# Optimization experiments

Measured on AMD Instinct MI355X. Metric: run time of the kernel, lower is better.

## Reference

```python
import jax, jax.numpy as jnp
import numpy as np

EMBED_DIM = 1024
NUM_HEADS = 16
HEAD_DIM = EMBED_DIM // NUM_HEADS
MAX_LEN = 1000  # default in RelativePositionalEncoding
B, T = 4, 1024


def setup_inputs() -> dict:
    key = jax.random.key(0)
    ks = jax.random.split(key, 12)
    s = 0.02
    d = EMBED_DIM
    return {
        "query": jax.random.normal(ks[0], (B, T, d), jnp.float32),
        "key": jax.random.normal(ks[1], (B, T, d), jnp.float32),
        "value": jax.random.normal(ks[2], (B, T, d), jnp.float32),
        "Wq": jax.random.normal(ks[3], (d, d), jnp.float32) * s,
        "bq": jnp.zeros((d,), jnp.float32),
        "Wk": jax.random.normal(ks[4], (d, d), jnp.float32) * s,
        "bk": jnp.zeros((d,), jnp.float32),
        "Wv": jax.random.normal(ks[5], (d, d), jnp.float32) * s,
        "bv": jnp.zeros((d,), jnp.float32),
        "Wo": jax.random.normal(ks[6], (d, d), jnp.float32) * s,
        "bo": jnp.zeros((d,), jnp.float32),
        "rel_emb": jax.random.normal(ks[7], (2 * MAX_LEN - 1, HEAD_DIM), jnp.float32) * s,
    }


def reference(query, key, value, Wq, bq, Wk, bk, Wv, bv, Wo, bo, rel_emb):
    Bq, Tq, C = query.shape
    H, hd = NUM_HEADS, HEAD_DIM
    # projections -> [B, H, T, hd]
    q = (query @ Wq.T + bq).reshape(Bq, Tq, H, hd).transpose(0, 2, 1, 3)
    k = (key @ Wk.T + bk).reshape(Bq, Tq, H, hd).transpose(0, 2, 1, 3)
    v = (value @ Wv.T + bv).reshape(Bq, Tq, H, hd).transpose(0, 2, 1, 3)
    # content scores [B, H, T, T]
    attn_scores = jnp.einsum('bhtd,bhsd->bhts', q, k)
    # relative positional embedding gather: E[t, s] = rel_emb[clamp(s - t + max_len - 1)]
    pos = jnp.arange(Tq)
    idx = jnp.clip(pos[None, :] - pos[:, None] + MAX_LEN - 1, 0, 2 * MAX_LEN - 2)
    E = rel_emb[idx]  # [T, T, hd]
    # NOTE: original uses raw (unprojected) query reshaped into heads for rel-pos scores
    rpe_q = query.transpose(1, 0, 2).reshape(Tq, Bq * H, hd)  # [T, B*H, hd]
    rpe = jnp.einsum('tnd,tsd->nts', rpe_q, E).reshape(Bq, H, Tq, Tq)
    # faithful to original: divide by scale = hd**-0.5 (i.e. multiply by sqrt(hd))
    scale = hd ** (-0.5)
    attn = (attn_scores + rpe) / scale
    attn_weights = jax.nn.softmax(attn, axis=-1)
    out = jnp.einsum('bhts,bhsd->bhtd', attn_weights, v)
    out = out.transpose(0, 2, 1, 3).reshape(Bq, Tq, C)
    return out @ Wo.T + bo
```

## Files before the change

kernel.cpp:

```cpp
#include <hip/hip_runtime.h>
#include <math.h>

typedef _Float16 h16;
typedef __attribute__((ext_vector_type(4))) _Float16 half4;
typedef __attribute__((ext_vector_type(8))) _Float16 half8;
typedef __attribute__((ext_vector_type(4))) float f32x4;

#define AS1 __attribute__((address_space(1)))
#define AS3 __attribute__((address_space(3)))
#define MFMA16(a, b, c) __builtin_amdgcn_mfma_f32_16x16x32_f16((a), (b), (c), 0, 0, 0)

__device__ __forceinline__ float ex2(float x) {
  return __builtin_amdgcn_exp2f(x);
}

template <int CTRL>
__device__ __forceinline__ float dppf(float x) {
  return __int_as_float(__builtin_amdgcn_update_dpp(
      0, __float_as_int(x), CTRL, 0xF, 0xF, true));
}
__device__ __forceinline__ float rmax16(float x) {
  x = fmaxf(x, dppf<0xB1>(x));
  x = fmaxf(x, dppf<0x4E>(x));
  x = fmaxf(x, dppf<0x124>(x));
  x = fmaxf(x, dppf<0x128>(x));
  return x;
}
__device__ __forceinline__ float rsum16(float x) {
  x += dppf<0xB1>(x);
  x += dppf<0x4E>(x);
  x += dppf<0x124>(x);
  x += dppf<0x128>(x);
  return x;
}

__global__ __launch_bounds__(256) void convert(
    const float* __restrict__ q, const float* __restrict__ k,
    const float* __restrict__ v, const float* __restrict__ Wq,
    const float* __restrict__ Wk, const float* __restrict__ Wv,
    const float* __restrict__ Wo, const float* __restrict__ rel, h16* q16c,
    h16* k16c, h16* v16c, h16* Wq16, h16* Wk16, h16* Wv16, h16* Wo16,
    h16* relb) {
  const int i = blockIdx.x * 256 + threadIdx.x;
  if (i >= 4226304) return;
  const float* src;
  h16* dst;
  int off;
  if (i < 1048576) {
    src = q; dst = q16c; off = i;
  } else if (i < 2097152) {
    src = k; dst = k16c; off = i - 1048576;
  } else if (i < 3145728) {
    src = v; dst = v16c; off = i - 2097152;
  } else if (i < 3407872) {
    src = Wq; dst = Wq16; off = i - 3145728;
  } else if (i < 3670016) {
    src = Wk; dst = Wk16; off = i - 3407872;
  } else if (i < 3932160) {
    src = Wv; dst = Wv16; off = i - 3670016;
  } else if (i < 4194304) {
    src = Wo; dst = Wo16; off = i - 3932160;
  } else {
    off = i - 4194304;
    half4 hv = (half4){(h16)0.f, (h16)0.f, (h16)0.f, (h16)0.f};
    if (off < 31984) {
      float4 f = *(const float4*)(rel + (size_t)off * 4);
      hv = (half4){(h16)f.x, (h16)f.y, (h16)f.z, (h16)f.w};
    }
    *(half4*)(relb + (size_t)off * 4) = hv;
    return;
  }
  float4 f = *(const float4*)(src + (size_t)off * 4);
  *(half4*)(dst + (size_t)off * 4) =
      (half4){(h16)f.x, (h16)f.y, (h16)f.z, (h16)f.w};
}

template <int MODE>
__device__ __forceinline__ void gemm128_body(const h16* __restrict__ A,
                                             const h16* __restrict__ Bt,
                                             const float* __restrict__ bias,
                                             h16* __restrict__ outp) {
  __shared__ alignas(16) h16 As[128 * 64];
  __shared__ alignas(16) h16 Bs[128 * 64];
  const int tid = threadIdx.x;
  const int wave = tid >> 6;
  const int lane = tid & 63;
  const int wm = wave >> 1, wn = wave & 1;
  const int tm0 = blockIdx.x * 128, tn0 = blockIdx.y * 128;
  const int lrow = lane & 15;
  const int kq = lane >> 4;

  f32x4 acc[4][4];
#pragma unroll
  for (int i = 0; i < 4; ++i)
#pragma unroll
    for (int j = 0; j < 4; ++j) acc[i][j] = (f32x4){0.f, 0.f, 0.f, 0.f};

  for (int k0 = 0; k0 < 1024; k0 += 64) {
    __syncthreads();
#pragma unroll
    for (int p = 0; p < 4; ++p) {
      const int a = (wave * 4 + p) * 64 + lane;
      const int row = a >> 3;
      const int c = (a & 7) ^ (row & 7);
      __builtin_amdgcn_global_load_lds(
          (const AS1 void*)(A + (size_t)(tm0 + row) * 1024 + k0 + c * 8),
          (AS3 void*)(As + (wave * 4 + p) * 512), 16, 0, 0);
      __builtin_amdgcn_global_load_lds(
          (const AS1 void*)(Bt + (size_t)(tn0 + row) * 1024 + k0 + c * 8),
          (AS3 void*)(Bs + (wave * 4 + p) * 512), 16, 0, 0);
    }
    __syncthreads();
#pragma unroll
    for (int ks2 = 0; ks2 < 2; ++ks2) {
      const int cu = ((ks2 * 4 + kq) ^ (lrow & 7)) << 3;
      half8 af[4], bf[4];
#pragma unroll
      for (int i = 0; i < 4; ++i)
        af[i] = *(const half8*)(As + (wm * 64 + i * 16 + lrow) * 64 + cu);
#pragma unroll
      for (int j = 0; j < 4; ++j)
        bf[j] = *(const half8*)(Bs + (wn * 64 + j * 16 + lrow) * 64 + cu);
#pragma unroll
      for (int i = 0; i < 4; ++i)
#pragma unroll
        for (int j = 0; j < 4; ++j)
          acc[i][j] = MFMA16(af[i], bf[j], acc[i][j]);
    }
  }

#pragma unroll
  for (int j = 0; j < 4; ++j) {
    const int n = tn0 + wn * 64 + j * 16 + lrow;
    const float bval = bias[n];
#pragma unroll
    for (int i = 0; i < 4; ++i) {
      const int rowb = wm * 64 + i * 16 + (lane >> 4) * 4;
#pragma unroll
      for (int r = 0; r < 4; ++r) {
        const int m = tm0 + rowb + r;
        const float val = acc[i][j][r] + bval;
        const int b = m >> 10, t = m & 1023, hh = n >> 6, d = n & 63;
        if (MODE == 0) {
          outp[((size_t)((b << 4) + hh) << 16) + (t << 6) + d] = (h16)val;
        } else {
          outp[(((size_t)((b << 4) + hh) * 64 + d) << 10) + t] = (h16)val;
        }
      }
    }
  }
}

__global__ __launch_bounds__(256) void qkv_gemm(
    const h16* q16c, const h16* k16c, const h16* v16c, const h16* Wq16,
    const h16* Wk16, const h16* Wv16, const float* bq, const float* bk,
    const float* bv, h16* q16, h16* k16, h16* vt16) {
  const int z = blockIdx.z;
  const h16* A = (z == 0) ? q16c : (z == 1) ? k16c : v16c;
  const h16* Bt = (z == 0) ? Wq16 : (z == 1) ? Wk16 : Wv16;
  const float* bias = (z == 0) ? bq : (z == 1) ? bk : bv;
  if (z == 2)
    gemm128_body<1>(A, Bt, bias, vt16);
  else
    gemm128_body<0>(A, Bt, bias, (z == 0) ? q16 : k16);
}

__global__ __launch_bounds__(256) void out_gemm(const h16* __restrict__ A,
                                                const h16* __restrict__ Bt,
                                                const float* __restrict__ bo,
                                                float* __restrict__ out) {
  __shared__ alignas(16) h16 As[64 * 64];
  __shared__ alignas(16) h16 Bs[128 * 64];
  const int tid = threadIdx.x;
  const int wave = tid >> 6;
  const int lane = tid & 63;
  const int wm = wave >> 1, wn = wave & 1;
  const int tm0 = blockIdx.x * 64, tn0 = blockIdx.y * 128;
  const int lrow = lane & 15;
  const int kq = lane >> 4;

  f32x4 acc[2][4];
#pragma unroll
  for (int i = 0; i < 2; ++i)
#pragma unroll
    for (int j = 0; j < 4; ++j) acc[i][j] = (f32x4){0.f, 0.f, 0.f, 0.f};

  for (int k0 = 0; k0 < 1024; k0 += 64) {
    __syncthreads();
#pragma unroll
    for (int p = 0; p < 2; ++p) {
      const int a = (wave * 2 + p) * 64 + lane;
      const int row = a >> 3;
      const int c = (a & 7) ^ (row & 7);
      __builtin_amdgcn_global_load_lds(
          (const AS1 void*)(A + (size_t)(tm0 + row) * 1024 + k0 + c * 8),
          (AS3 void*)(As + (wave * 2 + p) * 512), 16, 0, 0);
    }
#pragma unroll
    for (int p = 0; p < 4; ++p) {
      const int a = (wave * 4 + p) * 64 + lane;
      const int row = a >> 3;
      const int c = (a & 7) ^ (row & 7);
      __builtin_amdgcn_global_load_lds(
          (const AS1 void*)(Bt + (size_t)(tn0 + row) * 1024 + k0 + c * 8),
          (AS3 void*)(Bs + (wave * 4 + p) * 512), 16, 0, 0);
    }
    __syncthreads();
#pragma unroll
    for (int ks2 = 0; ks2 < 2; ++ks2) {
      const int cu = ((ks2 * 4 + kq) ^ (lrow & 7)) << 3;
      half8 af[2], bf[4];
#pragma unroll
      for (int i = 0; i < 2; ++i)
        af[i] = *(const half8*)(As + (wm * 32 + i * 16 + lrow) * 64 + cu);
#pragma unroll
      for (int j = 0; j < 4; ++j)
        bf[j] = *(const half8*)(Bs + (wn * 64 + j * 16 + lrow) * 64 + cu);
#pragma unroll
      for (int i = 0; i < 2; ++i)
#pragma unroll
        for (int j = 0; j < 4; ++j)
          acc[i][j] = MFMA16(af[i], bf[j], acc[i][j]);
    }
  }

#pragma unroll
  for (int j = 0; j < 4; ++j) {
    const int n = tn0 + wn * 64 + j * 16 + lrow;
    const float bval = bo[n];
#pragma unroll
    for (int i = 0; i < 2; ++i) {
      const int rowb = wm * 32 + i * 16 + kq * 4;
#pragma unroll
      for (int r = 0; r < 4; ++r) {
        const int m = tm0 + rowb + r;
        out[(size_t)m * 1024 + n] = acc[i][j][r] + bval;
      }
    }
  }
}

__global__ __launch_bounds__(256, 4) void attn_mfma(
    const h16* __restrict__ q16, const h16* __restrict__ k16,
    const h16* __restrict__ vt16, const h16* __restrict__ q16c,
    const h16* __restrict__ relb, h16* __restrict__ ao) {
  __shared__ alignas(16) h16 Kh[4096];
  __shared__ alignas(16) h16 Rl[8192];
  __shared__ alignas(16) h16 VtS[4096];
  __shared__ alignas(16) h16 Ps[4096];

  const int bid = blockIdx.x;
  const int ttile = bid & 15;
  const int bh = bid >> 4;
  const int b = bh >> 4, h = bh & 15;
  const int t0 = ttile << 6;
  const int tid = threadIdx.x;
  const int w = tid >> 6;
  const int lane = tid & 63;
  const int l15 = lane & 15;
  const int kq = lane >> 4;

  const int tq = t0 + w * 16 + l15;
  half8 aq[2], arq[2];
#pragma unroll
  for (int ks = 0; ks < 2; ++ks) {
    aq[ks] =
        *(const half8*)(q16 + ((size_t)bh * 1024 + tq) * 64 + kq * 8 + ks * 32);
    arq[ks] = *(const half8*)(q16c + ((size_t)(b * 1024 + tq)) * 1024 + h * 64 +
                              kq * 8 + ks * 32);
  }

  float m2[4], ls[4];
  f32x4 O[4];
#pragma unroll
  for (int r = 0; r < 4; ++r) {
    m2[r] = -1e30f;
    ls[r] = 0.f;
  }
#pragma unroll
  for (int db = 0; db < 4; ++db) O[db] = (f32x4){0.f, 0.f, 0.f, 0.f};

  const int trow = w * 16 + kq * 4;

  for (int s0 = 0; s0 < 1024; s0 += 64) {
    __syncthreads();

#pragma unroll
    for (int p = 0; p < 2; ++p) {
      const int a = (w * 2 + p) * 64 + lane;
      const int row = a >> 3;
      const int c = (a & 7) ^ (row & 7);
      __builtin_amdgcn_global_load_lds(
          (const AS1 void*)(k16 + ((size_t)(bh * 1024 + s0 + row)) * 64 +
                            c * 8),
          (AS3 void*)(Kh + (w * 2 + p) * 512), 16, 0, 0);
    }
#pragma unroll
    for (int p = 0; p < 2; ++p) {
      const int a = (w * 2 + p) * 64 + lane;
      const int row = a >> 3;
      const int c = (a & 7) ^ (row & 7);
      __builtin_amdgcn_global_load_lds(
          (const AS1 void*)(vt16 + ((size_t)(bh * 64 + row)) * 1024 + s0 +
                            c * 8),
          (AS3 void*)(VtS + (w * 2 + p) * 512), 16, 0, 0);
    }
    const int base = s0 - t0 + 999 - 63;
#pragma unroll
    for (int p = 0; p < 4; ++p) {
      const int a = (w * 4 + p) * 64 + lane;
      const int row = a >> 3;
      const int c = (a & 7) ^ (row & 7);
      int ridx = base + row;
      ridx = ridx < 0 ? 0 : (ridx > 1998 ? 1998 : ridx);
      __builtin_amdgcn_global_load_lds(
          (const AS1 void*)(relb + (size_t)ridx * 64 + c * 8),
          (AS3 void*)(Rl + (w * 4 + p) * 512), 16, 0, 0);
    }
    __syncthreads();

    __builtin_amdgcn_s_setprio(1);
    f32x4 S[4];
#pragma unroll
    for (int ns = 0; ns < 4; ++ns) {
      f32x4 s = (f32x4){0.f, 0.f, 0.f, 0.f};
      const int kr = ns * 16 + l15;
#pragma unroll
      for (int ks = 0; ks < 2; ++ks) {
        const int c = ((ks * 4 + kq) ^ (kr & 7)) << 3;
        s = MFMA16(aq[ks], *(const half8*)(Kh + kr * 64 + c), s);
      }
      S[ns] = s;
    }

    f32x4 G[5];
#pragma unroll
    for (int gi = 0; gi < 5; ++gi) {
      f32x4 g = (f32x4){0.f, 0.f, 0.f, 0.f};
      const int ur = (3 - w + gi) * 16 + l15;
#pragma unroll
      for (int ks = 0; ks < 2; ++ks) {
        const int c = ((ks * 4 + kq) ^ (ur & 7)) << 3;
        g = MFMA16(arq[ks], *(const half8*)(Rl + ur * 64 + c), g);
      }
      G[gi] = g;
    }
    __builtin_amdgcn_s_setprio(0);

    const float SC = 11.54156032711170727f;
#pragma unroll
    for (int r = 0; r < 4; ++r) {
      const int Cm = 15 - kq * 4 - r;
      const int sladdr = ((kq << 4) | ((l15 + Cm) & 15)) << 2;
      const bool nolap = (l15 >= Cm);
#pragma unroll
      for (int ns = 0; ns < 4; ++ns) {
        const float mv = nolap ? G[ns][r] : G[ns + 1][r];
        const float g = __int_as_float(
            __builtin_amdgcn_ds_bpermute(sladdr, __float_as_int(mv)));
        S[ns][r] = (S[ns][r] + g) * SC;
      }
    }

#pragma unroll
    for (int r = 0; r < 4; ++r) {
      float mx = fmaxf(fmaxf(S[0][r], S[1][r]), fmaxf(S[2][r], S[3][r]));
      mx = rmax16(mx);
      const float nm = fmaxf(m2[r], mx);
      const float al = ex2(m2[r] - nm);
      m2[r] = nm;
      const int t = trow + r;
      float rs = 0.f;
#pragma unroll
      for (int ns = 0; ns < 4; ++ns) {
        const float p = ex2(S[ns][r] - nm);
        rs += p;
        const int sl = ns * 16 + l15;
        Ps[t * 64 + (((sl >> 3) ^ (t & 7)) << 3) + (sl & 7)] = (h16)p;
      }
      rs = rsum16(rs);
      ls[r] = ls[r] * al + rs;
      O[0][r] *= al;
      O[1][r] *= al;
      O[2][r] *= al;
      O[3][r] *= al;
    }

    const int tp = w * 16 + l15;
    __builtin_amdgcn_s_setprio(1);
#pragma unroll
    for (int ks = 0; ks < 2; ++ks) {
      const int ca = ((ks * 4 + kq) ^ (tp & 7)) << 3;
      half8 pa = *(const half8*)(Ps + tp * 64 + ca);
#pragma unroll
      for (int db = 0; db < 4; ++db) {
        const int vr = db * 16 + l15;
        const int cb = ((ks * 4 + kq) ^ (vr & 7)) << 3;
        O[db] = MFMA16(pa, *(const half8*)(VtS + vr * 64 + cb), O[db]);
      }
    }
    __builtin_amdgcn_s_setprio(0);
  }

#pragma unroll
  for (int r = 0; r < 4; ++r) {
    const float inv = 1.f / ls[r];
    const int t = t0 + trow + r;
    h16* op = ao + ((size_t)(b * 1024 + t)) * 1024 + h * 64;
#pragma unroll
    for (int db = 0; db < 4; ++db) op[db * 16 + l15] = (h16)(O[db][r] * inv);
  }
}

extern "C" void kernel_launch(void* const* d_in, const int* in_sizes, int n_in,
                              void* d_out, int out_size, void* d_ws,
                              size_t ws_size, hipStream_t stream) {
  const float* query = (const float*)d_in[0];
  const float* key = (const float*)d_in[1];
  const float* value = (const float*)d_in[2];
  const float* Wq = (const float*)d_in[3];
  const float* bq = (const float*)d_in[4];
  const float* Wk = (const float*)d_in[5];
  const float* bk = (const float*)d_in[6];
  const float* Wv = (const float*)d_in[7];
  const float* bv = (const float*)d_in[8];
  const float* Wo = (const float*)d_in[9];
  const float* bo = (const float*)d_in[10];
  const float* rel = (const float*)d_in[11];

  char* ws = (char*)d_ws;
  h16* q16c = (h16*)ws;
  h16* k16c = (h16*)(ws + ((size_t)8 << 20));
  h16* v16c = (h16*)(ws + ((size_t)16 << 20));
  h16* Wq16 = (h16*)(ws + ((size_t)24 << 20));
  h16* Wk16 = (h16*)(ws + ((size_t)26 << 20));
  h16* Wv16 = (h16*)(ws + ((size_t)28 << 20));
  h16* Wo16 = (h16*)(ws + ((size_t)30 << 20));
  h16* q16 = (h16*)(ws + ((size_t)32 << 20));
  h16* k16 = (h16*)(ws + ((size_t)40 << 20));
  h16* vt16 = (h16*)(ws + ((size_t)48 << 20));
  h16* relb = (h16*)(ws + ((size_t)56 << 20));
  h16* ao = k16c;
  float* out = (float*)d_out;

  convert<<<16509, 256, 0, stream>>>(query, key, value, Wq, Wk, Wv, Wo, rel,
                                     q16c, k16c, v16c, Wq16, Wk16, Wv16, Wo16,
                                     relb);
  qkv_gemm<<<dim3(32, 8, 3), 256, 0, stream>>>(q16c, k16c, v16c, Wq16, Wk16,
                                               Wv16, bq, bk, bv, q16, k16,
                                               vt16);
  attn_mfma<<<1024, 256, 0, stream>>>(q16, k16, vt16, q16c, relb, ao);
  out_gemm<<<dim3(64, 8), 256, 0, stream>>>(ao, Wo16, bo, out);
}
```

Before: 252.7 us.

## Rewrite QKV GEMM as 256x256 double-buffered tile with interleaved prefetch

```diff
diff --git a/kernel.cpp b/kernel.cpp
--- a/kernel.cpp
+++ b/kernel.cpp
@@ -75,73 +75,109 @@
       (half4){(h16)f.x, (h16)f.y, (h16)f.z, (h16)f.w};
 }
 
-template <int MODE>
-__device__ __forceinline__ void gemm128_body(const h16* __restrict__ A,
-                                             const h16* __restrict__ Bt,
-                                             const float* __restrict__ bias,
-                                             h16* __restrict__ outp) {
-  __shared__ alignas(16) h16 As[128 * 64];
-  __shared__ alignas(16) h16 Bs[128 * 64];
+__global__ __launch_bounds__(512) void qkv_gemm(
+    const h16* q16c, const h16* k16c, const h16* v16c, const h16* Wq16,
+    const h16* Wk16, const h16* Wv16, const float* bq, const float* bk,
+    const float* bv, h16* q16, h16* k16, h16* vt16) {
+  __shared__ alignas(16) h16 AsB[2][16384];
+  __shared__ alignas(16) h16 BsB[2][16384];
+
+  const int z = blockIdx.z;
+  const h16* __restrict__ A = (z == 0) ? q16c : (z == 1) ? k16c : v16c;
+  const h16* __restrict__ Bt = (z == 0) ? Wq16 : (z == 1) ? Wk16 : Wv16;
+  const float* __restrict__ bias = (z == 0) ? bq : (z == 1) ? bk : bv;
+  h16* __restrict__ outp = (z == 0) ? q16 : (z == 1) ? k16 : vt16;
+  const int mode = (z == 2) ? 1 : 0;
+
   const int tid = threadIdx.x;
-  const int wave = tid >> 6;
+  const int w = tid >> 6;
   const int lane = tid & 63;
-  const int wm = wave >> 1, wn = wave & 1;
-  const int tm0 = blockIdx.x * 128, tn0 = blockIdx.y * 128;
-  const int lrow = lane & 15;
+  const int wm = w >> 2, wn = w & 3;
+  const int tm0 = blockIdx.x * 256, tn0 = blockIdx.y * 256;
+  const int l15 = lane & 15;
   const int kq = lane >> 4;
 
-  f32x4 acc[4][4];
-#pragma unroll
-  for (int i = 0; i < 4; ++i)
+  f32x4 acc[8][4];
+#pragma unroll
+  for (int i = 0; i < 8; ++i)
 #pragma unroll
     for (int j = 0; j < 4; ++j) acc[i][j] = (f32x4){0.f, 0.f, 0.f, 0.f};
 
-  for (int k0 = 0; k0 < 1024; k0 += 64) {
-    __syncthreads();
-#pragma unroll
-    for (int p = 0; p < 4; ++p) {
-      const int a = (wave * 4 + p) * 64 + lane;
-      const int row = a >> 3;
-      const int c = (a & 7) ^ (row & 7);
-      __builtin_amdgcn_global_load_lds(
-          (const AS1 void*)(A + (size_t)(tm0 + row) * 1024 + k0 + c * 8),
-          (AS3 void*)(As + (wave * 4 + p) * 512), 16, 0, 0);
-      __builtin_amdgcn_global_load_lds(
-          (const AS1 void*)(Bt + (size_t)(tn0 + row) * 1024 + k0 + c * 8),
-          (AS3 void*)(Bs + (wave * 4 + p) * 512), 16, 0, 0);
-    }
-    __syncthreads();
-#pragma unroll
-    for (int ks2 = 0; ks2 < 2; ++ks2) {
-      const int cu = ((ks2 * 4 + kq) ^ (lrow & 7)) << 3;
-      half8 af[4], bf[4];
-#pragma unroll
-      for (int i = 0; i < 4; ++i)
-        af[i] = *(const half8*)(As + (wm * 64 + i * 16 + lrow) * 64 + cu);
-#pragma unroll
-      for (int j = 0; j < 4; ++j)
-        bf[j] = *(const half8*)(Bs + (wn * 64 + j * 16 + lrow) * 64 + cu);
-#pragma unroll
-      for (int i = 0; i < 4; ++i)
-#pragma unroll
-        for (int j = 0; j < 4; ++j)
-          acc[i][j] = MFMA16(af[i], bf[j], acc[i][j]);
+  const auto stage_ht = [&](int b, int hq, int kt) {
+    const int k0 = kt * 64;
+    const h16* src = (hq < 2) ? A : Bt;
+    const int br = (hq < 2) ? tm0 : tn0;
+    h16* dst = ((hq < 2) ? AsB[b] : BsB[b]) + (hq & 1) * 8192;
+#pragma unroll
+    for (int p = 0; p < 2; ++p) {
+      const int u = (w * 2 + p) * 64 + lane;
+      const int row = (hq & 1) * 128 + (u >> 3);
+      const int c = (u & 7) ^ (row & 7);
+      __builtin_amdgcn_global_load_lds(
+          (const AS1 void*)(src + (size_t)(br + row) * 1024 + k0 + c * 8),
+          (AS3 void*)(dst + (w * 2 + p) * 512), 16, 0, 0);
+    }
+  };
+
+#pragma unroll
+  for (int hq = 0; hq < 4; ++hq) stage_ht(0, hq, 0);
+
+  for (int kt = 0; kt < 16; ++kt) {
+    asm volatile("s_waitcnt vmcnt(0)" ::: "memory");
+    __builtin_amdgcn_s_barrier();
+    const h16* As_ = AsB[kt & 1];
+    const h16* Bs_ = BsB[kt & 1];
+
+    half8 bf[4][2];
+#pragma unroll
+    for (int n = 0; n < 4; ++n)
+#pragma unroll
+      for (int kh = 0; kh < 2; ++kh) {
+        const int row = wn * 64 + n * 16 + l15;
+        const int cu = ((kh * 4 + kq) ^ (row & 7)) << 3;
+        bf[n][kh] = *(const half8*)(Bs_ + row * 64 + cu);
+      }
+
+#pragma unroll
+    for (int q = 0; q < 4; ++q) {
+      half8 af[2][2];
+#pragma unroll
+      for (int m2 = 0; m2 < 2; ++m2)
+#pragma unroll
+        for (int kh = 0; kh < 2; ++kh) {
+          const int row = wm * 128 + (q * 2 + m2) * 16 + l15;
+          const int cu = ((kh * 4 + kq) ^ (row & 7)) << 3;
+          af[m2][kh] = *(const half8*)(As_ + row * 64 + cu);
+        }
+      if (kt + 1 < 16) stage_ht((kt + 1) & 1, q, kt + 1);
+      __builtin_amdgcn_s_barrier();
+      __builtin_amdgcn_s_setprio(1);
+#pragma unroll
+      for (int m2 = 0; m2 < 2; ++m2)
+#pragma unroll
+        for (int n = 0; n < 4; ++n)
+#pragma unroll
+          for (int kh = 0; kh < 2; ++kh)
+            acc[q * 2 + m2][n] =
+                MFMA16(af[m2][kh], bf[n][kh], acc[q * 2 + m2][n]);
+      __builtin_amdgcn_s_setprio(0);
+      if (q < 3) __builtin_amdgcn_s_barrier();
     }
   }
 
 #pragma unroll
   for (int j = 0; j < 4; ++j) {
-    const int n = tn0 + wn * 64 + j * 16 + lrow;
+    const int n = tn0 + wn * 64 + j * 16 + l15;
     const float bval = bias[n];
 #pragma unroll
-    for (int i = 0; i < 4; ++i) {
-      const int rowb = wm * 64 + i * 16 + (lane >> 4) * 4;
+    for (int i = 0; i < 8; ++i) {
+      const int rowb = wm * 128 + i * 16 + kq * 4;
 #pragma unroll
       for (int r = 0; r < 4; ++r) {
         const int m = tm0 + rowb + r;
         const float val = acc[i][j][r] + bval;
         const int b = m >> 10, t = m & 1023, hh = n >> 6, d = n & 63;
-        if (MODE == 0) {
+        if (mode == 0) {
           outp[((size_t)((b << 4) + hh) << 16) + (t << 6) + d] = (h16)val;
         } else {
           outp[(((size_t)((b << 4) + hh) * 64 + d) << 10) + t] = (h16)val;
@@ -149,20 +185,6 @@
       }
     }
   }
-}
-
-__global__ __launch_bounds__(256) void qkv_gemm(
-    const h16* q16c, const h16* k16c, const h16* v16c, const h16* Wq16,
-    const h16* Wk16, const h16* Wv16, const float* bq, const float* bk,
-    const float* bv, h16* q16, h16* k16, h16* vt16) {
-  const int z = blockIdx.z;
-  const h16* A = (z == 0) ? q16c : (z == 1) ? k16c : v16c;
-  const h16* Bt = (z == 0) ? Wq16 : (z == 1) ? Wk16 : Wv16;
-  const float* bias = (z == 0) ? bq : (z == 1) ? bk : bv;
-  if (z == 2)
-    gemm128_body<1>(A, Bt, bias, vt16);
-  else
-    gemm128_body<0>(A, Bt, bias, (z == 0) ? q16 : k16);
 }
 
 __global__ __launch_bounds__(256) void out_gemm(const h16* __restrict__ A,
@@ -446,7 +468,7 @@
   convert<<<16509, 256, 0, stream>>>(query, key, value, Wq, Wk, Wv, Wo, rel,
                                      q16c, k16c, v16c, Wq16, Wk16, Wv16, Wo16,
                                      relb);
-  qkv_gemm<<<dim3(32, 8, 3), 256, 0, stream>>>(q16c, k16c, v16c, Wq16, Wk16,
+  qkv_gemm<<<dim3(16, 4, 3), 512, 0, stream>>>(q16c, k16c, v16c, Wq16, Wk16,
                                                Wv16, bq, bk, bv, q16, k16,
                                                vt16);
   attn_mfma<<<1024, 256, 0, stream>>>(q16, k16, vt16, q16c, relb, ao);
```

Result: slower. 260.0 us (+2.9%).

## Reuse overlapping rel-emb rows via ring buffer and lazily rescale softmax

Applied to the files above, without the earlier changes.

```diff
diff --git a/kernel.cpp b/kernel.cpp
--- a/kernel.cpp
+++ b/kernel.cpp
@@ -135,7 +135,7 @@
     const float bval = bias[n];
 #pragma unroll
     for (int i = 0; i < 4; ++i) {
-      const int rowb = wm * 64 + i * 16 + (lane >> 4) * 4;
+      const int rowb = wm * 64 + i * 16 + kq * 4;
 #pragma unroll
       for (int r = 0; r < 4; ++r) {
         const int m = tm0 + rowb + r;
@@ -282,6 +282,22 @@
 
   const int trow = w * 16 + kq * 4;
 
+  {
+    const int base0 = 936 - t0;
+#pragma unroll
+    for (int p = 0; p < 2; ++p) {
+      const int cw = w * 2 + p;
+      const int a = cw * 64 + lane;
+      const int lr = a >> 3;
+      const int c = (a & 7) ^ (lr & 7);
+      int ridx = base0 + lr;
+      ridx = ridx < 0 ? 0 : (ridx > 1998 ? 1998 : ridx);
+      __builtin_amdgcn_global_load_lds(
+          (const AS1 void*)(relb + (size_t)ridx * 64 + c * 8),
+          (AS3 void*)(Rl + cw * 512), 16, 0, 0);
+    }
+  }
+
   for (int s0 = 0; s0 < 1024; s0 += 64) {
     __syncthreads();
 
@@ -305,17 +321,20 @@
                             c * 8),
           (AS3 void*)(VtS + (w * 2 + p) * 512), 16, 0, 0);
     }
-    const int base = s0 - t0 + 999 - 63;
-#pragma unroll
-    for (int p = 0; p < 4; ++p) {
-      const int a = (w * 4 + p) * 64 + lane;
-      const int row = a >> 3;
-      const int c = (a & 7) ^ (row & 7);
-      int ridx = base + row;
+    const int base = s0 - t0 + 936;
+    const int roff = s0 & 64;
+#pragma unroll
+    for (int p = 0; p < 2; ++p) {
+      const int cw = w * 2 + p;
+      const int a = cw * 64 + lane;
+      const int lr = a >> 3;
+      const int c = (a & 7) ^ (lr & 7);
+      int ridx = base + 64 + lr;
       ridx = ridx < 0 ? 0 : (ridx > 1998 ? 1998 : ridx);
+      const int pb = (64 + cw * 8 + roff) & 127;
       __builtin_amdgcn_global_load_lds(
           (const AS1 void*)(relb + (size_t)ridx * 64 + c * 8),
-          (AS3 void*)(Rl + (w * 4 + p) * 512), 16, 0, 0);
+          (AS3 void*)(Rl + pb * 64), 16, 0, 0);
     }
     __syncthreads();
 
@@ -338,10 +357,11 @@
     for (int gi = 0; gi < 5; ++gi) {
       f32x4 g = (f32x4){0.f, 0.f, 0.f, 0.f};
       const int ur = (3 - w + gi) * 16 + l15;
+      const int pr = (ur + roff) & 127;
 #pragma unroll
       for (int ks = 0; ks < 2; ++ks) {
         const int c = ((ks * 4 + kq) ^ (ur & 7)) << 3;
-        g = MFMA16(arq[ks], *(const half8*)(Rl + ur * 64 + c), g);
+        g = MFMA16(arq[ks], *(const half8*)(Rl + pr * 64 + c), g);
       }
       G[gi] = g;
     }
@@ -366,9 +386,16 @@
     for (int r = 0; r < 4; ++r) {
       float mx = fmaxf(fmaxf(S[0][r], S[1][r]), fmaxf(S[2][r], S[3][r]));
       mx = rmax16(mx);
-      const float nm = fmaxf(m2[r], mx);
-      const float al = ex2(m2[r] - nm);
-      m2[r] = nm;
+      if (mx - m2[r] > 11.5f) {
+        const float al = ex2(m2[r] - mx);
+        m2[r] = mx;
+        ls[r] *= al;
+        O[0][r] *= al;
+        O[1][r] *= al;
+        O[2][r] *= al;
+        O[3][r] *= al;
+      }
+      const float nm = m2[r];
       const int t = trow + r;
       float rs = 0.f;
 #pragma unroll
@@ -379,11 +406,7 @@
         Ps[t * 64 + (((sl >> 3) ^ (t & 7)) << 3) + (sl & 7)] = (h16)p;
       }
       rs = rsum16(rs);
-      ls[r] = ls[r] * al + rs;
-      O[0][r] *= al;
-      O[1][r] *= al;
-      O[2][r] *= al;
-      O[3][r] *= al;
+      ls[r] += rs;
     }
 
     const int tp = w * 16 + l15;
```

After: 298.4 us. 18.1% more time.
